# Kernel optimization log

Measured on AMD Instinct MI355X. Metric: run time of the kernel, lower is better.

The kernel has to match this reference:

```python
import jax, jax.numpy as jnp
import numpy as np

PERIOD = 15          # hardcoded in the torch module's forward: STL(series, 15)
N_SEASONAL = 7       # statsmodels STL default seasonal smoother length
N_TREND = 29         # smallest odd >= 1.5*p/(1-1.5/7) = 28.64 -> 29 (statsmodels default)
N_LOWPASS = 17       # smallest odd > period (statsmodels default)
N_INNER = 2          # statsmodels: robust=False -> 2 inner iterations, 0 outer


def _loess_matrix(n, q, ts):
    """Dense linear operator for degree-1 LOESS smoothing of a length-n series
    evaluated at (possibly out-of-range) integer positions ts. Non-robust LOESS is
    linear in y, so smoothing == matmul with this constant matrix."""
    M = np.zeros((len(ts), n), dtype=np.float64)
    qq = min(q, n)
    for i, t in enumerate(ts):
        left = int(np.clip(t - (q - 1) // 2, 0, n - qq))
        right = left + qq - 1
        h = max(t - left, right - t)
        if q > n:
            h += (q - n) / 2.0
        xs = np.arange(left, right + 1, dtype=np.float64)
        w = np.clip(1.0 - (np.abs(xs - t) / h) ** 3, 0.0, None) ** 3  # tricube
        w = w / w.sum()
        xbar = (w * xs).sum()
        var = (w * (xs - xbar) ** 2).sum()
        a = w.copy()
        if var > 1e-12:  # degree-1 local linear fit; fall back to deg-0 if degenerate
            a = w * (1.0 + (t - xbar) * (xs - xbar) / var)
        M[i, left:right + 1] = a
    return M.astype(np.float32)


def _ma(x, k):
    """Moving average of window k along last axis (valid mode)."""
    cs = jnp.cumsum(x, axis=-1)
    cs = jnp.concatenate([jnp.zeros(x.shape[:-1] + (1,), x.dtype), cs], axis=-1)
    return (cs[..., k:] - cs[..., :-k]) / k


def setup_inputs() -> dict:
    key = jax.random.key(0)
    x = jax.random.normal(key, (128, 480, 256), dtype=jnp.float32)  # [B, T, C]
    return {"x": x}


def reference(x):
    B, T, Cc = x.shape
    p = PERIOD
    n_sub = T // p  # cycle-subseries length; T chosen divisible by period

    # Constant LOESS smoothing operators (numpy, baked in as jit constants)
    M_seas = jnp.asarray(_loess_matrix(n_sub, N_SEASONAL, np.arange(-1, n_sub + 1)))  # (n_sub+2, n_sub)
    M_lp = jnp.asarray(_loess_matrix(T, N_LOWPASS, np.arange(T)))                     # (T, T)
    M_trend = jnp.asarray(_loess_matrix(T, N_TREND, np.arange(T)))                    # (T, T)

    y = jnp.transpose(x, (0, 2, 1))  # [B, C, T]
    trend = jnp.zeros_like(y)
    seasonal = jnp.zeros_like(y)

    for _ in range(N_INNER):  # STL inner loop (Cleveland 1990, non-robust)
        # 1. detrend
        D = y - trend
        # 2. cycle-subseries LOESS smoothing, extended one period each side
        Dsub = D.reshape(B, Cc, n_sub, p)                      # subseries along axis 2
        Cext = jnp.einsum('sn,bcnp->bcsp', M_seas, Dsub)       # [B,C,n_sub+2,p]
        Cext = Cext.reshape(B, Cc, (n_sub + 2) * p)            # time order, length T+2p
        # 3. low-pass: MA(p) x2, MA(3), then LOESS(n_l)
        lp = _ma(_ma(_ma(Cext, p), p), 3)                      # length T
        L = jnp.einsum('tn,bcn->bct', M_lp, lp)
        # 4. seasonal = smoothed subseries (center T) minus low-pass
        seasonal = Cext[..., p:p + T] - L
        # 5+6. deseasonalize and trend LOESS
        trend = jnp.einsum('tn,bcn->bct', M_trend, y - seasonal)

    resid = y - seasonal - trend
    seas_plus_resid = jnp.transpose(seasonal + resid, (0, 2, 1))  # [B, T, C]
    trend_out = jnp.transpose(trend, (0, 2, 1))
    return (seas_plus_resid, trend_out)
```

## Files before the change

kernel.cpp:

```cpp
#include <hip/hip_runtime.h>
#include <hip/hip_bf16.h>
#include <stdint.h>

#define TLEN 480
#define NB 128
#define NC 256

typedef short bf16x8 __attribute__((ext_vector_type(8)));
typedef float f32x4 __attribute__((ext_vector_type(4)));
typedef unsigned short u16;

__device__ inline u16 f2bf(float f) {
    union { float f; uint32_t u; } v; v.f = f;
    uint32_t u = v.u;
    return (u16)((u + 0x7fffu + ((u >> 16) & 1u)) >> 16);
}

__device__ int loess_w(int t, int n, int q, float* out) {
    int left = t - (q - 1) / 2;
    if (left < 0) left = 0;
    if (left > n - q) left = n - q;
    int right = left + q - 1;
    int h = (t - left) > (right - t) ? (t - left) : (right - t);
    double w[29];
    double wsum = 0.0;
    for (int i = 0; i < q; ++i) {
        double dist = fabs((double)(left + i - t)) / (double)h;
        double u = 1.0 - dist * dist * dist;
        if (u < 0.0) u = 0.0;
        double wv = u * u * u;
        w[i] = wv; wsum += wv;
    }
    for (int i = 0; i < q; ++i) w[i] /= wsum;
    double xbar = 0.0;
    for (int i = 0; i < q; ++i) xbar += w[i] * (double)(left + i);
    double var = 0.0;
    for (int i = 0; i < q; ++i) { double d = (double)(left + i) - xbar; var += w[i] * d * d; }
    if (var > 1e-12) {
        double tb = (double)t - xbar;
        for (int i = 0; i < q; ++i) {
            double d = (double)(left + i) - xbar;
            out[i] = (float)(w[i] * (1.0 + tb * d / var));
        }
    } else {
        for (int i = 0; i < q; ++i) out[i] = (float)w[i];
    }
    return left;
}

__global__ void k_loess(float* Ms, float* w3, float* MlpC, float* MtC) {
    int gid = blockIdx.x * 256 + threadIdx.x;
    if (gid < 34) {
        float wl[7];
        int left = loess_w(gid - 1, 32, 7, wl);
        float* row = Ms + gid * 32;
        #pragma unroll
        for (int i = 0; i < 32; ++i) row[i] = 0.0f;
        for (int i = 0; i < 7; ++i) row[left + i] = wl[i];
    } else if (gid < 514) {
        int t = gid - 34;
        float wl[17];
        loess_w(t, TLEN, 17, wl);
        for (int i = 0; i < 17; ++i) MlpC[t * 17 + i] = wl[i];
    } else if (gid < 994) {
        int t = gid - 514;
        float wl[29];
        loess_w(t, TLEN, 29, wl);
        for (int i = 0; i < 29; ++i) MtC[t * 29 + i] = wl[i];
    } else if (gid == 994) {
        for (int d = 0; d <= 30; ++d) {
            int cnt = 0;
            for (int c = 0; c < 3; ++c)
                for (int a = 0; a < 15; ++a) {
                    int b = d - a - c;
                    if (b >= 0 && b < 15) cnt++;
                }
            w3[d] = (float)((double)cnt / 675.0);
        }
    }
}

__global__ void k_S(const float* __restrict__ Ms, const float* __restrict__ w3,
                    const float* __restrict__ MlpC, float* __restrict__ S) {
    int id = blockIdx.x * 256 + threadIdx.x;
    if (id >= TLEN * TLEN) return;
    int t = id / TLEN, u = id - t * TLEN;
    int nu = u / 15, ju = u - nu * 15;
    int slp = t - 8;
    if (slp < 0) slp = 0;
    if (slp > TLEN - 17) slp = TLEN - 17;
    float acc = 0.0f;
    for (int k = 0; k < 17; ++k) {
        int i = slp + k;
        int s_lo = (i - ju + 14) / 15;
        float g = 0.0f;
        #pragma unroll
        for (int ds = 0; ds < 3; ++ds) {
            int s = s_lo + ds;
            int d = s * 15 + ju - i;
            if (s >= 0 && s < 34 && d >= 0 && d <= 30)
                g += Ms[s * 32 + nu] * w3[d];
        }
        acc += MlpC[t * 17 + k] * g;
    }
    float val = -acc;
    if (t % 15 == ju) val += Ms[(1 + t / 15) * 32 + nu];
    S[id] = val;
}

__global__ void k_VU(const float* __restrict__ MtC, const float* __restrict__ S,
                     float* __restrict__ U, float* __restrict__ V) {
    int id = blockIdx.x * 256 + threadIdx.x;
    if (id >= TLEN * TLEN) return;
    int t = id / TLEN, u = id - t * TLEN;
    int st = t - 14;
    if (st < 0) st = 0;
    if (st > TLEN - 29) st = TLEN - 29;
    float acc = 0.0f;
    for (int k = 0; k < 29; ++k)
        acc += MtC[t * 29 + k] * S[(size_t)(st + k) * TLEN + u];
    float mt = (u >= st && u < st + 29) ? MtC[t * 29 + (u - st)] : 0.0f;
    V[id] = acc;
    U[id] = mt - acc;
}

__global__ void k_A(const float* __restrict__ U, const float* __restrict__ V,
                    u16* __restrict__ Abf) {
    __shared__ float Vs[16][17];
    __shared__ float Us[16][17];
    int tx = threadIdx.x, ty = threadIdx.y;
    int u = blockIdx.x * 16 + tx;
    int t = blockIdx.y * 16 + ty;
    float acc = 0.0f;
    for (int kt = 0; kt < 30; ++kt) {
        Vs[ty][tx] = V[(size_t)t * TLEN + kt * 16 + tx];
        Us[ty][tx] = U[(size_t)(kt * 16 + ty) * TLEN + u];
        __syncthreads();
        #pragma unroll
        for (int e = 0; e < 16; ++e) acc += Vs[ty][e] * Us[e][tx];
        __syncthreads();
    }
    Abf[(size_t)t * TLEN + u] = f2bf(U[(size_t)t * TLEN + u] + acc);
}

__global__ void k_tr(const float* __restrict__ x, u16* __restrict__ Xt) {
    __shared__ u16 Tt[32 * 36];
    int b = blockIdx.z, s0 = blockIdx.y * 32, c0 = blockIdx.x * 32;
    int i = threadIdx.x;
    int r = i >> 3, cg = i & 7;
    float4 v = *(const float4*)(x + (((size_t)b * TLEN + s0 + r) * NC + c0 + cg * 4));
    Tt[(cg * 4 + 0) * 36 + r] = f2bf(v.x);
    Tt[(cg * 4 + 1) * 36 + r] = f2bf(v.y);
    Tt[(cg * 4 + 2) * 36 + r] = f2bf(v.z);
    Tt[(cg * 4 + 3) * 36 + r] = f2bf(v.w);
    __syncthreads();
    int cl = i >> 3, ch = i & 7;
    ushort4 o = *(const ushort4*)&Tt[cl * 36 + ch * 4];
    *(ushort4*)(Xt + (((size_t)b * NC + c0 + cl) * TLEN + s0 + ch * 4)) = o;
}

__global__ __launch_bounds__(256, 4)
void k_gemm(const u16* __restrict__ A, const u16* __restrict__ Xt,
            const float* __restrict__ x, float* __restrict__ out0, float* __restrict__ out1) {
    int b = blockIdx.x;
    int t0 = blockIdx.y * 48;
    int tid = threadIdx.x;
    int wave = tid >> 6, lane = tid & 63;
    int lane15 = lane & 15, quad = lane >> 4;
    int cw = wave * 64;

    const u16* ap[4];
    #pragma unroll
    for (int i = 0; i < 4; ++i)
        ap[i] = Xt + ((size_t)b * NC + cw + i * 16 + lane15) * TLEN + quad * 8;
    const u16* bp[3];
    #pragma unroll
    for (int j = 0; j < 3; ++j)
        bp[j] = A + (size_t)(t0 + j * 16 + lane15) * TLEN + quad * 8;

    f32x4 acc[4][3] = {};
    for (int k0 = 0; k0 < TLEN; k0 += 32) {
        bf16x8 af[4], bfr[3];
        #pragma unroll
        for (int i = 0; i < 4; ++i) af[i] = *(const bf16x8*)(ap[i] + k0);
        #pragma unroll
        for (int j = 0; j < 3; ++j) bfr[j] = *(const bf16x8*)(bp[j] + k0);
        #pragma unroll
        for (int i = 0; i < 4; ++i)
            #pragma unroll
            for (int j = 0; j < 3; ++j)
                acc[i][j] = __builtin_amdgcn_mfma_f32_16x16x32_bf16(af[i], bfr[j], acc[i][j], 0, 0, 0);
    }

    #pragma unroll
    for (int i = 0; i < 4; ++i) {
        #pragma unroll
        for (int j = 0; j < 3; ++j) {
            int t = t0 + j * 16 + lane15;
            int c = cw + i * 16 + quad * 4;
            size_t base = ((size_t)b * TLEN + t) * NC + c;
            float4 xv = *(const float4*)(x + base);
            float4 tv = make_float4(acc[i][j][0], acc[i][j][1], acc[i][j][2], acc[i][j][3]);
            *(float4*)(out1 + base) = tv;
            *(float4*)(out0 + base) = make_float4(xv.x - tv.x, xv.y - tv.y, xv.z - tv.z, xv.w - tv.w);
        }
    }
}

extern "C" void kernel_launch(void* const* d_in, const int* in_sizes, int n_in,
                              void* d_out, int out_size, void* d_ws, size_t ws_size,
                              hipStream_t stream) {
    const float* x = (const float*)d_in[0];
    float* out0 = (float*)d_out;
    float* out1 = (float*)d_out + (size_t)NB * TLEN * NC;

    char* ws = (char*)d_ws;
    size_t oXt  = 0;
    size_t oMs  = 31457280;
    size_t oW3  = oMs + 4352;
    size_t oLpC = oW3 + 128;
    size_t oMtC = oLpC + 32640;
    size_t oS   = oMtC + 55680;
    size_t oU   = oS + 921600;
    size_t oV   = oU + 921600;
    size_t oA   = oV + 921600;

    u16*   Xt   = (u16*)(ws + oXt);
    float* Ms   = (float*)(ws + oMs);
    float* w3   = (float*)(ws + oW3);
    float* MlpC = (float*)(ws + oLpC);
    float* MtC  = (float*)(ws + oMtC);
    float* S    = (float*)(ws + oS);
    float* U    = (float*)(ws + oU);
    float* V    = (float*)(ws + oV);
    u16*   Abf  = (u16*)(ws + oA);

    k_loess<<<4, 256, 0, stream>>>(Ms, w3, MlpC, MtC);
    k_S<<<900, 256, 0, stream>>>(Ms, w3, MlpC, S);
    k_VU<<<900, 256, 0, stream>>>(MtC, S, U, V);
    k_A<<<dim3(30, 30), dim3(16, 16), 0, stream>>>(U, V, Abf);
    k_tr<<<dim3(8, 15, NB), 256, 0, stream>>>(x, Xt);
    k_gemm<<<dim3(NB, 10), 256, 0, stream>>>(Abf, Xt, x, out0, out1);
}
```

Before: 289.5 us.

## Fuse input transpose/bf16 conversion into GEMM via swizzled LDS staging

Removes the separate transpose kernel and its bf16 workspace. The GEMM now loads fp32 x tiles directly, packs them to bf16 with a byte-permute and writes them transposed into a swizzled shared-memory buffer before the MFMA loop. Output stores become nontemporal. This saves one pass over x and a write/read of Xt. In exchange, each of the 10 t-blocks per batch re-reads and re-converts the full x slice, adds two barriers per k-step, and the LDS footprint may limit occupancy.

Result: no change. 287.8 us (-0.6%).

```diff
diff --git a/kernel.cpp b/kernel.cpp
--- a/kernel.cpp
+++ b/kernel.cpp
@@ -9,11 +9,16 @@
 typedef short bf16x8 __attribute__((ext_vector_type(8)));
 typedef float f32x4 __attribute__((ext_vector_type(4)));
 typedef unsigned short u16;
+typedef unsigned int u32;
 
 __device__ inline u16 f2bf(float f) {
     union { float f; uint32_t u; } v; v.f = f;
     uint32_t u = v.u;
     return (u16)((u + 0x7fffu + ((u >> 16) & 1u)) >> 16);
+}
+
+__device__ inline u32 pack2bf(float lo, float hi) {
+    return __builtin_amdgcn_perm(__float_as_uint(hi), __float_as_uint(lo), 0x07060302u);
 }
 
 __device__ int loess_w(int t, int n, int q, float* out) {
@@ -143,25 +148,10 @@
     Abf[(size_t)t * TLEN + u] = f2bf(U[(size_t)t * TLEN + u] + acc);
 }
 
-__global__ void k_tr(const float* __restrict__ x, u16* __restrict__ Xt) {
-    __shared__ u16 Tt[32 * 36];
-    int b = blockIdx.z, s0 = blockIdx.y * 32, c0 = blockIdx.x * 32;
-    int i = threadIdx.x;
-    int r = i >> 3, cg = i & 7;
-    float4 v = *(const float4*)(x + (((size_t)b * TLEN + s0 + r) * NC + c0 + cg * 4));
-    Tt[(cg * 4 + 0) * 36 + r] = f2bf(v.x);
-    Tt[(cg * 4 + 1) * 36 + r] = f2bf(v.y);
-    Tt[(cg * 4 + 2) * 36 + r] = f2bf(v.z);
-    Tt[(cg * 4 + 3) * 36 + r] = f2bf(v.w);
-    __syncthreads();
-    int cl = i >> 3, ch = i & 7;
-    ushort4 o = *(const ushort4*)&Tt[cl * 36 + ch * 4];
-    *(ushort4*)(Xt + (((size_t)b * NC + c0 + cl) * TLEN + s0 + ch * 4)) = o;
-}
-
 __global__ __launch_bounds__(256, 4)
-void k_gemm(const u16* __restrict__ A, const u16* __restrict__ Xt,
-            const float* __restrict__ x, float* __restrict__ out0, float* __restrict__ out1) {
+void k_gemm(const u16* __restrict__ A, const float* __restrict__ x,
+            float* __restrict__ out0, float* __restrict__ out1) {
+    __shared__ u16 Xs[NC * 40];
     int b = blockIdx.x;
     int t0 = blockIdx.y * 48;
     int tid = threadIdx.x;
@@ -169,20 +159,50 @@
     int lane15 = lane & 15, quad = lane >> 4;
     int cw = wave * 64;
 
-    const u16* ap[4];
-    #pragma unroll
-    for (int i = 0; i < 4; ++i)
-        ap[i] = Xt + ((size_t)b * NC + cw + i * 16 + lane15) * TLEN + quad * 8;
     const u16* bp[3];
     #pragma unroll
     for (int j = 0; j < 3; ++j)
         bp[j] = A + (size_t)(t0 + j * 16 + lane15) * TLEN + quad * 8;
 
+    int kkq = tid >> 5;
+    int wq  = tid & 31;
+    int kq_sw = kkq ^ ((wq & 3) << 1);
+
+    const float* xbase = x + (size_t)b * TLEN * NC;
+
     f32x4 acc[4][3] = {};
-    for (int k0 = 0; k0 < TLEN; k0 += 32) {
+    for (int s = 0; s < 15; ++s) {
+        int k0 = s * 32;
+        if (s) __syncthreads();
+        #pragma unroll
+        for (int it = 0; it < 2; ++it) {
+            int c0 = wq * 4 + it * 128;
+            const float* xp = xbase + (size_t)(k0 + kkq * 4) * NC + c0;
+            float4 r0 = *(const float4*)(xp);
+            float4 r1 = *(const float4*)(xp + NC);
+            float4 r2 = *(const float4*)(xp + 2 * NC);
+            float4 r3 = *(const float4*)(xp + 3 * NC);
+            u32* base32 = (u32*)Xs;
+            int o0 = c0 * 20 + kq_sw * 2;
+            uint2 w;
+            w.x = pack2bf(r0.x, r1.x); w.y = pack2bf(r2.x, r3.x);
+            *(uint2*)(base32 + o0) = w;
+            w.x = pack2bf(r0.y, r1.y); w.y = pack2bf(r2.y, r3.y);
+            *(uint2*)(base32 + o0 + 20) = w;
+            w.x = pack2bf(r0.z, r1.z); w.y = pack2bf(r2.z, r3.z);
+            *(uint2*)(base32 + o0 + 40) = w;
+            w.x = pack2bf(r0.w, r1.w); w.y = pack2bf(r2.w, r3.w);
+            *(uint2*)(base32 + o0 + 60) = w;
+        }
+        __syncthreads();
+
         bf16x8 af[4], bfr[3];
         #pragma unroll
-        for (int i = 0; i < 4; ++i) af[i] = *(const bf16x8*)(ap[i] + k0);
+        for (int i = 0; i < 4; ++i) {
+            int c = cw + i * 16 + lane15;
+            int qp = quad ^ ((c >> 2) & 3);
+            af[i] = *(const bf16x8*)&Xs[c * 40 + qp * 8];
+        }
         #pragma unroll
         for (int j = 0; j < 3; ++j) bfr[j] = *(const bf16x8*)(bp[j] + k0);
         #pragma unroll
@@ -199,10 +219,11 @@
             int t = t0 + j * 16 + lane15;
             int c = cw + i * 16 + quad * 4;
             size_t base = ((size_t)b * TLEN + t) * NC + c;
-            float4 xv = *(const float4*)(x + base);
-            float4 tv = make_float4(acc[i][j][0], acc[i][j][1], acc[i][j][2], acc[i][j][3]);
-            *(float4*)(out1 + base) = tv;
-            *(float4*)(out0 + base) = make_float4(xv.x - tv.x, xv.y - tv.y, xv.z - tv.z, xv.w - tv.w);
+            f32x4 xv = *(const f32x4*)(x + base);
+            f32x4 tv = acc[i][j];
+            __builtin_nontemporal_store(tv, (f32x4*)(out1 + base));
+            f32x4 sv = xv - tv;
+            __builtin_nontemporal_store(sv, (f32x4*)(out0 + base));
         }
     }
 }
@@ -215,8 +236,7 @@
     float* out1 = (float*)d_out + (size_t)NB * TLEN * NC;
 
     char* ws = (char*)d_ws;
-    size_t oXt  = 0;
-    size_t oMs  = 31457280;
+    size_t oMs  = 0;
     size_t oW3  = oMs + 4352;
     size_t oLpC = oW3 + 128;
     size_t oMtC = oLpC + 32640;
@@ -225,7 +245,6 @@
     size_t oV   = oU + 921600;
     size_t oA   = oV + 921600;
 
-    u16*   Xt   = (u16*)(ws + oXt);
     float* Ms   = (float*)(ws + oMs);
     float* w3   = (float*)(ws + oW3);
     float* MlpC = (float*)(ws + oLpC);
@@ -239,6 +258,5 @@
     k_S<<<900, 256, 0, stream>>>(Ms, w3, MlpC, S);
     k_VU<<<900, 256, 0, stream>>>(MtC, S, U, V);
     k_A<<<dim3(30, 30), dim3(16, 16), 0, stream>>>(U, V, Abf);
-    k_tr<<<dim3(8, 15, NB), 256, 0, stream>>>(x, Xt);
-    k_gemm<<<dim3(NB, 10), 256, 0, stream>>>(Abf, Xt, x, out0, out1);
-}
+    k_gemm<<<dim3(NB, 10), 256, 0, stream>>>(Abf, x, out0, out1);
+}
```
